# Performance work log

Measured on AMD Instinct MI355X. Metric: run time of the kernel, lower is better.

## Reference

```python
import jax, jax.numpy as jnp
import numpy as np

L = 2
GRID_RES = 0.01
ATOL = 0.01
RTOL = 1e-5  # torch.isclose default rtol


def _grad_matrices(filtration, bar, sample_pts):
    # filtration: [S,2] simplex (x,y) filtration values
    # bar:        [P,R] bar length per sample point, per rank
    # sample_pts: [P,2] center points
    S = filtration.shape[0]
    P, R = bar.shape
    shift = jnp.arange(-L, L + 1, dtype=filtration.dtype)          # [5]
    fx = filtration[:, 0]
    fy = filtration[:, 1]
    ptx = sample_pts[:, 0]
    pty = sample_pts[:, 1]
    scale = bar + GRID_RES                                          # [P,R]
    line_x = shift[None, None, :] * scale[:, :, None] + ptx[:, None, None]  # [P,R,5]
    line_y = shift[None, None, :] * scale[:, :, None] + pty[:, None, None]  # [P,R,5]
    last_x = line_x[:, :, -1]                                       # [P,R]
    last_y = line_y[:, :, -1]                                       # [P,R]
    # torch.isclose(a, b, atol): |a-b| <= atol + rtol*|b|
    tol_x = ATOL + RTOL * jnp.abs(fx)                               # [S]
    tol_y = ATOL + RTOL * jnp.abs(fy)
    close_x = jnp.any(jnp.abs(line_x[:, :, None, :] - fx[None, None, :, None])
                      <= tol_x[None, None, :, None], axis=-1)       # [P,R,S]
    close_y = jnp.any(jnp.abs(line_y[:, :, None, :] - fy[None, None, :, None])
                      <= tol_y[None, None, :, None], axis=-1)       # [P,R,S]
    fsum = fx + fy                                                  # [S]
    psum = (ptx + pty)[:, None, None]                               # [P,1,1]
    below = fsum[None, None, :] < psum                              # [P,1,S]
    above = fsum[None, None, :] > psum
    cond_x = close_x & (fy[None, None, :] <= last_y[:, :, None])    # [P,R,S]
    cond_y = close_y & (fx[None, None, :] <= last_x[:, :, None])
    lower_x = cond_x & below
    upper_x = cond_x & above
    lower_y = cond_y & below
    upper_y = cond_y & above
    gx = jnp.where(upper_x, 1.0, jnp.where(lower_x, -1.0, 0.0))     # [P,R,S]
    gy = jnp.where(upper_y, 1.0, jnp.where(lower_y, -1.0, 0.0))
    # interleave x/y per simplex: columns (2s, 2s+1)
    gm = jnp.stack([gx, gy], axis=-1).reshape(P, R, 2 * S).transpose(1, 0, 2)  # [R,P,2S]
    any_s = lambda m: jnp.any(m, axis=2)                            # [P,R]
    cx = jnp.where(any_s(upper_x), -1.0, jnp.where(any_s(lower_x), 1.0, 0.0))
    cy = jnp.where(any_s(upper_y), -1.0, jnp.where(any_s(lower_y), 1.0, 0.0))
    gc = jnp.stack([cx, cy], axis=-1).transpose(1, 0, 2)            # [R,P,2]
    return gm, gc


def setup_inputs() -> dict:
    key = jax.random.key(0)
    k1, k2, k3, k4 = jax.random.split(key, 4)
    S, P, R = 2000, 2500, 5
    filtration = jax.random.uniform(k1, (S, 2), dtype=jnp.float32)
    bars_h0 = jax.random.uniform(k2, (P, R), dtype=jnp.float32)
    bars_h1 = jax.random.uniform(k3, (P, R), dtype=jnp.float32)
    sample_pts = jax.random.uniform(k4, (P, 2), dtype=jnp.float32)
    return {"filtration": filtration, "bars_h0": bars_h0,
            "bars_h1": bars_h1, "sample_pts": sample_pts}


def reference(filtration, bars_h0, bars_h1, sample_pts):
    # moveSimplices.forward: passes bars through and builds the sparse
    # per-point gradient matrices (the dominant compute) for H0 and H1.
    gm0, gc0 = _grad_matrices(filtration, bars_h0, sample_pts)
    gm1, gc1 = _grad_matrices(filtration, bars_h1, sample_pts)
    out = jnp.stack([bars_h0, bars_h1])  # forward returns (bars[0], bars[1])
    return out, gm0, gc0, gm1, gc1
```

## Files before the change

### kernel.cpp

```cpp
#include <hip/hip_runtime.h>

#define S 2000
#define P 2500
#define R 5
#define HALF (S / 2)
#define NIT 16

typedef float floatx4 __attribute__((ext_vector_type(4)));

__global__ __launch_bounds__(256) void grad_kernel(
    const float* __restrict__ filtration,
    const float* __restrict__ bars0,
    const float* __restrict__ bars1,
    const float* __restrict__ sample_pts,
    float* __restrict__ out,
    float* __restrict__ gm0, float* __restrict__ gc0,
    float* __restrict__ gm1, float* __restrict__ gc1)
{
    int job = blockIdx.x * 4 + (threadIdx.x >> 6);
    int lane = threadIdx.x & 63;
    int h = job / (R * P);
    int rem = job - h * (R * P);
    int r = rem / P;
    int p = rem - r * P;

    const float* bars = h ? bars1 : bars0;
    float* gm = h ? gm1 : gm0;
    float* gc = h ? gc1 : gc0;

    float bar = bars[p * R + r];
    float scale = bar + 0.01f;
    float ptx = sample_pts[2 * p];
    float pty = sample_pts[2 * p + 1];
    float psum = ptx + pty;

    float lxk[5], lyk[5];
#pragma unroll
    for (int k = 0; k < 5; ++k) {
        float ks = (float)(k - 2) * scale;
        lxk[k] = ks + ptx;
        lyk[k] = ks + pty;
    }
    float lastx = lxk[4];
    float lasty = lyk[4];

    if (lane == 0) out[(size_t)h * P * R + p * R + r] = bar;

    const floatx4* filt4 = (const floatx4*)filtration;
    float* gmrow = gm + ((size_t)r * P + p) * (size_t)(2 * S);

    float axmax = 0.f, axmin = 0.f, aymax = 0.f, aymin = 0.f;

#pragma unroll
    for (int it = 0; it < NIT; ++it) {
        int j = lane + 64 * it;
        if (it < NIT - 1 || j < HALF) {
            floatx4 f = filt4[j];
            floatx4 o;
            {
                float fx = f.x, fy = f.y;
                float tolx = __fadd_rn(0.01f, __fmul_rn(1e-5f, __builtin_fabsf(fx)));
                float toly = __fadd_rn(0.01f, __fmul_rn(1e-5f, __builtin_fabsf(fy)));
                bool cx = false, cy = false;
#pragma unroll
                for (int k = 0; k < 5; ++k) {
                    cx = cx || (__builtin_fabsf(lxk[k] - fx) <= tolx);
                    cy = cy || (__builtin_fabsf(lyk[k] - fy) <= toly);
                }
                float fsum = fx + fy;
                bool above = fsum > psum;
                bool below = fsum < psum;
                float sgn = above ? 1.0f : (below ? -1.0f : 0.0f);
                o.x = (cx && (fy <= lasty)) ? sgn : 0.0f;
                o.y = (cy && (fx <= lastx)) ? sgn : 0.0f;
            }
            {
                float fx = f.z, fy = f.w;
                float tolx = __fadd_rn(0.01f, __fmul_rn(1e-5f, __builtin_fabsf(fx)));
                float toly = __fadd_rn(0.01f, __fmul_rn(1e-5f, __builtin_fabsf(fy)));
                bool cx = false, cy = false;
#pragma unroll
                for (int k = 0; k < 5; ++k) {
                    cx = cx || (__builtin_fabsf(lxk[k] - fx) <= tolx);
                    cy = cy || (__builtin_fabsf(lyk[k] - fy) <= toly);
                }
                float fsum = fx + fy;
                bool above = fsum > psum;
                bool below = fsum < psum;
                float sgn = above ? 1.0f : (below ? -1.0f : 0.0f);
                o.z = (cx && (fy <= lasty)) ? sgn : 0.0f;
                o.w = (cy && (fx <= lastx)) ? sgn : 0.0f;
            }
            axmax = fmaxf(axmax, fmaxf(o.x, o.z));
            axmin = fminf(axmin, fminf(o.x, o.z));
            aymax = fmaxf(aymax, fmaxf(o.y, o.w));
            aymin = fminf(aymin, fminf(o.y, o.w));
            *(floatx4*)(gmrow + (size_t)j * 4) = o;
        }
    }

    bool anyUx = __any(axmax > 0.f);
    bool anyLx = __any(axmin < 0.f);
    bool anyUy = __any(aymax > 0.f);
    bool anyLy = __any(aymin < 0.f);
    if (lane == 0) {
        float cxv = anyUx ? -1.0f : (anyLx ? 1.0f : 0.0f);
        float cyv = anyUy ? -1.0f : (anyLy ? 1.0f : 0.0f);
        float2 v = make_float2(cxv, cyv);
        *(float2*)(gc + ((size_t)r * P + p) * 2) = v;
    }
}

extern "C" void kernel_launch(void* const* d_in, const int* in_sizes, int n_in,
                              void* d_out, int out_size, void* d_ws, size_t ws_size,
                              hipStream_t stream) {
    const float* filtration = (const float*)d_in[0];
    const float* bars_h0    = (const float*)d_in[1];
    const float* bars_h1    = (const float*)d_in[2];
    const float* sample_pts = (const float*)d_in[3];

    float* out = (float*)d_out;
    float* o_stack = out;
    float* gm0     = o_stack + (size_t)2 * P * R;
    float* gc0     = gm0 + (size_t)R * P * 2 * S;
    float* gm1     = gc0 + (size_t)R * P * 2;
    float* gc1     = gm1 + (size_t)R * P * 2 * S;

    grad_kernel<<<(2 * R * P) / 4, 256, 0, stream>>>(filtration, bars_h0, bars_h1, sample_pts,
                                                     o_stack, gm0, gc0, gm1, gc1);
}
```

Baseline: 86.65 us.

## Process all five ranks per wave to reuse filtration loads and per-simplex math

Each wavefront now handles one (h, p) pair and loops over all R ranks, so each filtration vector is loaded once and its tolerance and sign terms are computed once, then reused for five output rows. The launch shrinks to 2*P/4 blocks. The any-of-five closeness test becomes a min of absolute differences compared against the tolerance, and the job index is made wave-uniform with readfirstlane. The kernel is dominated by output writes (about 200MB), so the gain is limited to the compute and load side. Register pressure and per-wave store streams both rise.

```diff
diff --git a/kernel.cpp b/kernel.cpp
--- a/kernel.cpp
+++ b/kernel.cpp
@@ -17,97 +17,126 @@
     float* __restrict__ gm0, float* __restrict__ gc0,
     float* __restrict__ gm1, float* __restrict__ gc1)
 {
-    int job = blockIdx.x * 4 + (threadIdx.x >> 6);
+    int job = __builtin_amdgcn_readfirstlane(blockIdx.x * 4 + (threadIdx.x >> 6));
     int lane = threadIdx.x & 63;
-    int h = job / (R * P);
-    int rem = job - h * (R * P);
-    int r = rem / P;
-    int p = rem - r * P;
+    int h = job / P;
+    int p = job - h * P;
 
     const float* bars = h ? bars1 : bars0;
     float* gm = h ? gm1 : gm0;
     float* gc = h ? gc1 : gc0;
 
-    float bar = bars[p * R + r];
-    float scale = bar + 0.01f;
     float ptx = sample_pts[2 * p];
     float pty = sample_pts[2 * p + 1];
     float psum = ptx + pty;
 
-    float lxk[5], lyk[5];
+    float barv[R], lx[R][5], ly[R][5];
 #pragma unroll
-    for (int k = 0; k < 5; ++k) {
-        float ks = (float)(k - 2) * scale;
-        lxk[k] = ks + ptx;
-        lyk[k] = ks + pty;
+    for (int r = 0; r < R; ++r) {
+        float bar = bars[p * R + r];
+        barv[r] = bar;
+        float sc = bar + 0.01f;
+#pragma unroll
+        for (int k = 0; k < 5; ++k) {
+            float ks = (float)(k - 2) * sc;
+            lx[r][k] = ks + ptx;
+            ly[r][k] = ks + pty;
+        }
     }
-    float lastx = lxk[4];
-    float lasty = lyk[4];
 
-    if (lane == 0) out[(size_t)h * P * R + p * R + r] = bar;
+    if (lane == 0) {
+#pragma unroll
+        for (int r = 0; r < R; ++r)
+            out[(size_t)h * (P * R) + p * R + r] = barv[r];
+    }
 
     const floatx4* filt4 = (const floatx4*)filtration;
-    float* gmrow = gm + ((size_t)r * P + p) * (size_t)(2 * S);
 
-    float axmax = 0.f, axmin = 0.f, aymax = 0.f, aymin = 0.f;
+    float* gmr[R];
+#pragma unroll
+    for (int r = 0; r < R; ++r)
+        gmr[r] = gm + ((size_t)r * P + p) * (size_t)(2 * S);
+
+    float axmax[R], axmin[R], aymax[R], aymin[R];
+#pragma unroll
+    for (int r = 0; r < R; ++r) {
+        axmax[r] = 0.f; axmin[r] = 0.f; aymax[r] = 0.f; aymin[r] = 0.f;
+    }
 
 #pragma unroll
     for (int it = 0; it < NIT; ++it) {
         int j = lane + 64 * it;
         if (it < NIT - 1 || j < HALF) {
             floatx4 f = filt4[j];
-            floatx4 o;
-            {
-                float fx = f.x, fy = f.y;
-                float tolx = __fadd_rn(0.01f, __fmul_rn(1e-5f, __builtin_fabsf(fx)));
-                float toly = __fadd_rn(0.01f, __fmul_rn(1e-5f, __builtin_fabsf(fy)));
-                bool cx = false, cy = false;
+            float tolx0 = __fadd_rn(0.01f, __fmul_rn(1e-5f, __builtin_fabsf(f.x)));
+            float toly0 = __fadd_rn(0.01f, __fmul_rn(1e-5f, __builtin_fabsf(f.y)));
+            float tolx1 = __fadd_rn(0.01f, __fmul_rn(1e-5f, __builtin_fabsf(f.z)));
+            float toly1 = __fadd_rn(0.01f, __fmul_rn(1e-5f, __builtin_fabsf(f.w)));
+            float s0 = f.x + f.y;
+            float s1 = f.z + f.w;
+            float sgn0 = (s0 > psum) ? 1.0f : ((s0 < psum) ? -1.0f : 0.0f);
+            float sgn1 = (s1 > psum) ? 1.0f : ((s1 < psum) ? -1.0f : 0.0f);
+
 #pragma unroll
-                for (int k = 0; k < 5; ++k) {
-                    cx = cx || (__builtin_fabsf(lxk[k] - fx) <= tolx);
-                    cy = cy || (__builtin_fabsf(lyk[k] - fy) <= toly);
+            for (int r = 0; r < R; ++r) {
+                float lastx = lx[r][4], lasty = ly[r][4];
+                floatx4 o;
+                {
+                    float m = fminf(fminf(__builtin_fabsf(lx[r][0] - f.x),
+                                          __builtin_fabsf(lx[r][1] - f.x)),
+                                    fminf(__builtin_fabsf(lx[r][2] - f.x),
+                                          __builtin_fabsf(lx[r][3] - f.x)));
+                    m = fminf(m, __builtin_fabsf(lastx - f.x));
+                    float t = (m <= tolx0) ? sgn0 : 0.0f;
+                    o.x = (f.y <= lasty) ? t : 0.0f;
                 }
-                float fsum = fx + fy;
-                bool above = fsum > psum;
-                bool below = fsum < psum;
-                float sgn = above ? 1.0f : (below ? -1.0f : 0.0f);
-                o.x = (cx && (fy <= lasty)) ? sgn : 0.0f;
-                o.y = (cy && (fx <= lastx)) ? sgn : 0.0f;
+                {
+                    float m = fminf(fminf(__builtin_fabsf(ly[r][0] - f.y),
+                                          __builtin_fabsf(ly[r][1] - f.y)),
+                                    fminf(__builtin_fabsf(ly[r][2] - f.y),
+                                          __builtin_fabsf(ly[r][3] - f.y)));
+                    m = fminf(m, __builtin_fabsf(lasty - f.y));
+                    float t = (m <= toly0) ? sgn0 : 0.0f;
+                    o.y = (f.x <= lastx) ? t : 0.0f;
+                }
+                {
+                    float m = fminf(fminf(__builtin_fabsf(lx[r][0] - f.z),
+                                          __builtin_fabsf(lx[r][1] - f.z)),
+                                    fminf(__builtin_fabsf(lx[r][2] - f.z),
+                                          __builtin_fabsf(lx[r][3] - f.z)));
+                    m = fminf(m, __builtin_fabsf(lastx - f.z));
+                    float t = (m <= tolx1) ? sgn1 : 0.0f;
+                    o.z = (f.w <= lasty) ? t : 0.0f;
+                }
+                {
+                    float m = fminf(fminf(__builtin_fabsf(ly[r][0] - f.w),
+                                          __builtin_fabsf(ly[r][1] - f.w)),
+                                    fminf(__builtin_fabsf(ly[r][2] - f.w),
+                                          __builtin_fabsf(ly[r][3] - f.w)));
+                    m = fminf(m, __builtin_fabsf(lasty - f.w));
+                    float t = (m <= toly1) ? sgn1 : 0.0f;
+                    o.w = (f.z <= lastx) ? t : 0.0f;
+                }
+                axmax[r] = fmaxf(axmax[r], fmaxf(o.x, o.z));
+                axmin[r] = fminf(axmin[r], fminf(o.x, o.z));
+                aymax[r] = fmaxf(aymax[r], fmaxf(o.y, o.w));
+                aymin[r] = fminf(aymin[r], fminf(o.y, o.w));
+                *(floatx4*)(gmr[r] + (size_t)j * 4) = o;
             }
-            {
-                float fx = f.z, fy = f.w;
-                float tolx = __fadd_rn(0.01f, __fmul_rn(1e-5f, __builtin_fabsf(fx)));
-                float toly = __fadd_rn(0.01f, __fmul_rn(1e-5f, __builtin_fabsf(fy)));
-                bool cx = false, cy = false;
-#pragma unroll
-                for (int k = 0; k < 5; ++k) {
-                    cx = cx || (__builtin_fabsf(lxk[k] - fx) <= tolx);
-                    cy = cy || (__builtin_fabsf(lyk[k] - fy) <= toly);
-                }
-                float fsum = fx + fy;
-                bool above = fsum > psum;
-                bool below = fsum < psum;
-                float sgn = above ? 1.0f : (below ? -1.0f : 0.0f);
-                o.z = (cx && (fy <= lasty)) ? sgn : 0.0f;
-                o.w = (cy && (fx <= lastx)) ? sgn : 0.0f;
-            }
-            axmax = fmaxf(axmax, fmaxf(o.x, o.z));
-            axmin = fminf(axmin, fminf(o.x, o.z));
-            aymax = fmaxf(aymax, fmaxf(o.y, o.w));
-            aymin = fminf(aymin, fminf(o.y, o.w));
-            *(floatx4*)(gmrow + (size_t)j * 4) = o;
         }
     }
 
-    bool anyUx = __any(axmax > 0.f);
-    bool anyLx = __any(axmin < 0.f);
-    bool anyUy = __any(aymax > 0.f);
-    bool anyLy = __any(aymin < 0.f);
-    if (lane == 0) {
-        float cxv = anyUx ? -1.0f : (anyLx ? 1.0f : 0.0f);
-        float cyv = anyUy ? -1.0f : (anyLy ? 1.0f : 0.0f);
-        float2 v = make_float2(cxv, cyv);
-        *(float2*)(gc + ((size_t)r * P + p) * 2) = v;
+#pragma unroll
+    for (int r = 0; r < R; ++r) {
+        bool anyUx = __any(axmax[r] > 0.f);
+        bool anyLx = __any(axmin[r] < 0.f);
+        bool anyUy = __any(aymax[r] > 0.f);
+        bool anyLy = __any(aymin[r] < 0.f);
+        if (lane == 0) {
+            float cxv = anyUx ? -1.0f : (anyLx ? 1.0f : 0.0f);
+            float cyv = anyUy ? -1.0f : (anyLy ? 1.0f : 0.0f);
+            *(float2*)(gc + ((size_t)r * P + p) * 2) = make_float2(cxv, cyv);
+        }
     }
 }
 
@@ -126,6 +155,6 @@
     float* gm1     = gc0 + (size_t)R * P * 2;
     float* gc1     = gm1 + (size_t)R * P * 2 * S;
 
-    grad_kernel<<<(2 * R * P) / 4, 256, 0, stream>>>(filtration, bars_h0, bars_h1, sample_pts,
-                                                     o_stack, gm0, gc0, gm1, gc1);
+    grad_kernel<<<(2 * P) / 4, 256, 0, stream>>>(filtration, bars_h0, bars_h1, sample_pts,
+                                                 o_stack, gm0, gc0, gm1, gc1);
 }
```

Measured after the change: 102.8 us. 18.6% more time.
